# Kernel tuning notes

Measured on AMD Instinct MI355X. Metric: run time of the kernel, lower is better.

Reference implementation:

```python
import jax, jax.numpy as jnp
import numpy as np

N = 100000      # nodes
E = 1600000     # edges (avg degree 16)
IN_DIM = 64
H = 4           # num_heads
D = 32          # out_dim per head
NEG_SLOPE = 0.1


def setup_inputs() -> dict:
    key = jax.random.key(0)
    k_x, k_src, k_dst, k_w, k_fc, k_al, k_ar = jax.random.split(key, 7)
    x = jax.random.normal(k_x, (N, IN_DIM), dtype=jnp.float32)
    src = jax.random.randint(k_src, (E,), 0, N, dtype=jnp.int32)
    dst = jax.random.randint(k_dst, (E,), 0, N, dtype=jnp.int32)
    w = jax.random.uniform(k_w, (E,), dtype=jnp.float32)
    # xavier-ish init for learned params
    W_fc = jax.random.normal(k_fc, (IN_DIM, H * D), dtype=jnp.float32) * (2.0 / (IN_DIM + H * D)) ** 0.5
    attn_l = jax.random.normal(k_al, (1, H, D), dtype=jnp.float32) * 0.1
    attn_r = jax.random.normal(k_ar, (1, H, D), dtype=jnp.float32) * 0.1
    vt = jnp.zeros((1,), dtype=jnp.float32)  # unused by forward (as in the source)
    return {"vt": vt, "x": x, "src": src, "dst": dst, "w": w,
            "W_fc": W_fc, "attn_l": attn_l, "attn_r": attn_r}


def reference(vt, x, src, dst, w, W_fc, attn_l, attn_r):
    # node projection: [N, H, D]
    feat = (x @ W_fc).reshape(-1, H, D)
    el = jnp.sum(feat * attn_l, axis=-1)  # [N, H]
    er = jnp.sum(feat * attn_r, axis=-1)  # [N, H]
    # per-edge logits: u_add_v then leaky_relu, scaled by edge weight w
    e = el[src] + er[dst]                                   # [E, H]
    e = jnp.where(e >= 0, e, NEG_SLOPE * e)                 # leaky_relu
    e = w[:, None] * e                                      # [E, H]
    # edge softmax grouped by destination node (numerically stable)
    m = jax.ops.segment_max(e, dst, num_segments=N)         # [N, H]
    ex = jnp.exp(e - m[dst])                                # [E, H]
    den = jax.ops.segment_sum(ex, dst, num_segments=N)      # [N, H]
    a = ex / den[dst]                                       # [E, H]
    # message passing: u_mul_e -> sum over incoming edges
    msg = feat[src] * a[:, :, None]                         # [E, H, D]
    out = jax.ops.segment_sum(msg, dst, num_segments=N)     # [N, H, D]
    return out
```

## Files before the change

### kernel.cpp

```cpp
#include <hip/hip_runtime.h>
#include <math.h>

#define IN_DIM 64
#define HH 4
#define CC 128
#define NEG_SLOPE 0.1f

typedef __attribute__((ext_vector_type(8))) short short8;
typedef __attribute__((ext_vector_type(4))) float f32x4;

__device__ __forceinline__ float leaky(float v) { return v >= 0.f ? v : NEG_SLOPE * v; }

__device__ __forceinline__ unsigned f2bf(float f) {
  unsigned u = __float_as_uint(f);
  unsigned r = u + 0x7FFFu + ((u >> 16) & 1u);
  return r >> 16;
}

__global__ void k_prepw(const float* __restrict__ W, unsigned* __restrict__ wt) {
  int tid = blockIdx.x * 256 + threadIdx.x;
  if (tid >= 128 * 32) return;
  int n = tid >> 5;
  int r = tid & 31;
  int b = r >> 2, h = r & 3;
  int k = b * 8 + h * 2;
  unsigned lo = f2bf(W[k * CC + n]);
  unsigned hi = f2bf(W[(k + 1) * CC + n]);
  wt[n * 32 + (b ^ (n & 7)) * 4 + h] = lo | (hi << 16);
}

__global__ __launch_bounds__(256) void k_project(
    const float* __restrict__ x, const unsigned* __restrict__ wt,
    const float* __restrict__ attn_l, const float* __restrict__ attn_r,
    unsigned char* __restrict__ featQ, float* __restrict__ scale,
    float* __restrict__ el, float* __restrict__ er, int N)
{
  __shared__ unsigned Wlds[4096];
  __shared__ float Al[CC], Ar[CC];
  int t = threadIdx.x;
  {
    const uint4* s = (const uint4*)wt;
    uint4* d = (uint4*)Wlds;
#pragma unroll
    for (int i = 0; i < 4; ++i) d[t + 256 * i] = s[t + 256 * i];
  }
  if (t < CC) { Al[t] = attn_l[t]; Ar[t] = attn_r[t]; }
  __syncthreads();

  int lane = t & 63;
  int l4 = lane >> 4, l16 = lane & 15;
  int node = blockIdx.x * 64 + (t >> 6) * 16 + l16;
  bool valid = node < N;
  int nrow = valid ? node : 0;

  short8 bfr[2];
#pragma unroll
  for (int s = 0; s < 2; ++s) {
    const float4* xp = (const float4*)&x[(size_t)nrow * 64 + s * 32 + l4 * 8];
    float4 xa = xp[0], xb = xp[1];
    union { short8 v; unsigned u[4]; } pk;
    pk.u[0] = f2bf(xa.x) | (f2bf(xa.y) << 16);
    pk.u[1] = f2bf(xa.z) | (f2bf(xa.w) << 16);
    pk.u[2] = f2bf(xb.x) | (f2bf(xb.y) << 16);
    pk.u[3] = f2bf(xb.z) | (f2bf(xb.w) << 16);
    bfr[s] = pk.v;
  }

  f32x4 acc[8];
#pragma unroll
  for (int c = 0; c < 8; ++c) acc[c] = (f32x4){0.f, 0.f, 0.f, 0.f};

#pragma unroll
  for (int c = 0; c < 8; ++c) {
    int n0 = c * 16 + l16;
    int sw = n0 & 7;
#pragma unroll
    for (int s = 0; s < 2; ++s) {
      int b = s * 4 + l4;
      union { short8 v; uint4 q; } af;
      af.q = *(const uint4*)&Wlds[n0 * 32 + (b ^ sw) * 4];
      acc[c] = __builtin_amdgcn_mfma_f32_16x16x32_bf16(af.v, bfr[s], acc[c], 0, 0, 0);
    }
  }

  float mx = 0.f;
#pragma unroll
  for (int c = 0; c < 8; ++c) {
#pragma unroll
    for (int r = 0; r < 4; ++r) mx = fmaxf(mx, fabsf(acc[c][r]));
  }
  mx = fmaxf(mx, __shfl_xor(mx, 16, 64));
  mx = fmaxf(mx, __shfl_xor(mx, 32, 64));
  float mxs = fmaxf(mx, 1e-20f);
  float inv = 127.f / mxs;

  if (valid) {
#pragma unroll
    for (int c = 0; c < 8; ++c) {
      int q0 = __float2int_rn(acc[c][0] * inv) + 128;
      int q1 = __float2int_rn(acc[c][1] * inv) + 128;
      int q2 = __float2int_rn(acc[c][2] * inv) + 128;
      int q3 = __float2int_rn(acc[c][3] * inv) + 128;
      unsigned u = (unsigned)(q0 & 0xff) | ((unsigned)(q1 & 0xff) << 8) |
                   ((unsigned)(q2 & 0xff) << 16) | ((unsigned)(q3 & 0xff) << 24);
      *(unsigned*)&featQ[(size_t)node * 128 + c * 16 + l4 * 4] = u;
    }
    if (l4 == 0) scale[node] = mxs * (1.f / 127.f);
  }

  float pl[4], pr[4];
#pragma unroll
  for (int h = 0; h < 4; ++h) {
    float sl = 0.f, sr = 0.f;
#pragma unroll
    for (int ct = 0; ct < 2; ++ct) {
      int c = 2 * h + ct;
      int cb = c * 16 + l4 * 4;
#pragma unroll
      for (int r = 0; r < 4; ++r) {
        sl = fmaf(acc[c][r], Al[cb + r], sl);
        sr = fmaf(acc[c][r], Ar[cb + r], sr);
      }
    }
    sl += __shfl_xor(sl, 16, 64); sl += __shfl_xor(sl, 32, 64);
    sr += __shfl_xor(sr, 16, 64); sr += __shfl_xor(sr, 32, 64);
    pl[h] = sl; pr[h] = sr;
  }
  if (l4 == 0 && valid) {
    *(float4*)&el[(size_t)node * 4] = make_float4(pl[0], pl[1], pl[2], pl[3]);
    *(float4*)&er[(size_t)node * 4] = make_float4(pr[0], pr[1], pr[2], pr[3]);
  }
}

__global__ __launch_bounds__(256) void k_bhist(const int* __restrict__ dst,
                                               int* __restrict__ bcnt, int E, int NB) {
  __shared__ int lh[512];
  for (int i = threadIdx.x; i < NB; i += 256) lh[i] = 0;
  __syncthreads();
  int stride = gridDim.x * 256;
  for (int i = blockIdx.x * 256 + threadIdx.x; i < E; i += stride)
    atomicAdd(&lh[dst[i] >> 8], 1);
  __syncthreads();
  for (int i = threadIdx.x; i < NB; i += 256) {
    int c = lh[i];
    if (c) atomicAdd(&bcnt[i], c);
  }
}

__global__ __launch_bounds__(512) void k_bscan(const int* __restrict__ bcnt,
                                               int* __restrict__ gbase,
                                               int* __restrict__ gcursor, int NB) {
  __shared__ int sh[512];
  int t = threadIdx.x;
  int v = (t < NB) ? bcnt[t] : 0;
  sh[t] = v;
  __syncthreads();
  for (int off = 1; off < 512; off <<= 1) {
    int a = (t >= off) ? sh[t - off] : 0;
    __syncthreads();
    sh[t] += a;
    __syncthreads();
  }
  if (t < NB) {
    int e = sh[t] - v;
    gbase[t] = e;
    gcursor[t] = e;
  }
}

__global__ __launch_bounds__(512) void k_binA(const int* __restrict__ src,
                                              const int* __restrict__ dst,
                                              const float* __restrict__ w,
                                              int* __restrict__ gcursor,
                                              uint2* __restrict__ bkt, int E, int NB) {
  __shared__ int lh[512];
  __shared__ int lbase[512];
  int t = threadIdx.x;
  for (int i = t; i < NB; i += 512) lh[i] = 0;
  __syncthreads();
  long eb = (long)blockIdx.x * 8192;
  int b[16]; int r[16]; unsigned px[16]; unsigned pw[16];
#pragma unroll
  for (int i = 0; i < 16; ++i) {
    long e = eb + t + i * 512;
    bool v = e < E;
    int d = v ? dst[e] : 0;
    b[i] = d >> 8;
    px[i] = v ? ((unsigned)src[e] | ((unsigned)(d & 255) << 20)) : 0u;
    pw[i] = v ? ((const unsigned*)w)[e] : 0u;
    r[i] = v ? atomicAdd(&lh[b[i]], 1) : -1;
  }
  __syncthreads();
  for (int i = t; i < NB; i += 512) {
    int c = lh[i];
    lbase[i] = c ? atomicAdd(&gcursor[i], c) : 0;
  }
  __syncthreads();
#pragma unroll
  for (int i = 0; i < 16; ++i)
    if (r[i] >= 0) bkt[lbase[b[i]] + r[i]] = make_uint2(px[i], pw[i]);
}

__global__ __launch_bounds__(256) void k_binB(const uint2* __restrict__ bkt,
                                              const int* __restrict__ bcnt,
                                              const int* __restrict__ gbase,
                                              int* __restrict__ offs,
                                              int2* __restrict__ sp,
                                              int N, int E, int NB) {
  __shared__ int lh[256], sc[256], lcur[256];
  int b = blockIdx.x;
  int t = threadIdx.x;
  int base_b = gbase[b];
  int cnt_b = bcnt[b];
  lh[t] = 0;
  __syncthreads();
  for (int e = t; e < cnt_b; e += 256) {
    uint2 p = bkt[base_b + e];
    atomicAdd(&lh[(p.x >> 20) & 255], 1);
  }
  __syncthreads();
  int v = lh[t];
  sc[t] = v;
  __syncthreads();
  for (int off = 1; off < 256; off <<= 1) {
    int a = (t >= off) ? sc[t - off] : 0;
    __syncthreads();
    sc[t] += a;
    __syncthreads();
  }
  int excl = sc[t] - v;
  lcur[t] = excl;
  int n0 = b << 8;
  if (n0 + t < N) offs[n0 + t] = base_b + excl;
  if (b == NB - 1 && t == 0) offs[N] = E;
  __syncthreads();
  for (int e = t; e < cnt_b; e += 256) {
    uint2 p = bkt[base_b + e];
    int d = (p.x >> 20) & 255;
    int pos = atomicAdd(&lcur[d], 1);
    sp[base_b + pos] = make_int2((int)(p.x & 0xFFFFFu), (int)p.y);
  }
}

__device__ __forceinline__ void fma16(float* acc, float& ka, float a, uint4 f) {
  ka += a;
  acc[0]  = fmaf(a, (float)( f.x        & 0xffu), acc[0]);
  acc[1]  = fmaf(a, (float)((f.x >> 8 ) & 0xffu), acc[1]);
  acc[2]  = fmaf(a, (float)((f.x >> 16) & 0xffu), acc[2]);
  acc[3]  = fmaf(a, (float)( f.x >> 24        ), acc[3]);
  acc[4]  = fmaf(a, (float)( f.y        & 0xffu), acc[4]);
  acc[5]  = fmaf(a, (float)((f.y >> 8 ) & 0xffu), acc[5]);
  acc[6]  = fmaf(a, (float)((f.y >> 16) & 0xffu), acc[6]);
  acc[7]  = fmaf(a, (float)( f.y >> 24        ), acc[7]);
  acc[8]  = fmaf(a, (float)( f.z        & 0xffu), acc[8]);
  acc[9]  = fmaf(a, (float)((f.z >> 8 ) & 0xffu), acc[9]);
  acc[10] = fmaf(a, (float)((f.z >> 16) & 0xffu), acc[10]);
  acc[11] = fmaf(a, (float)( f.z >> 24        ), acc[11]);
  acc[12] = fmaf(a, (float)( f.w        & 0xffu), acc[12]);
  acc[13] = fmaf(a, (float)((f.w >> 8 ) & 0xffu), acc[13]);
  acc[14] = fmaf(a, (float)((f.w >> 16) & 0xffu), acc[14]);
  acc[15] = fmaf(a, (float)( f.w >> 24        ), acc[15]);
}

__global__ __launch_bounds__(256) void k_aggregate(
    const int* __restrict__ offs, const int2* __restrict__ sp,
    const float* __restrict__ el, const float* __restrict__ er,
    const float* __restrict__ scale, const unsigned char* __restrict__ featQ,
    float* __restrict__ out, int N)
{
  __shared__ int    s_lds[4][64];
  __shared__ float4 a_lds[4][64];

  int t = threadIdx.x;
  int lane = t & 63, wv = t >> 6;
  int half = lane >> 5, l32 = lane & 31;
  int n = blockIdx.x * 8 + wv * 2 + half;
  if (n >= N) return;

  int off0 = offs[n], off1 = offs[n + 1];
  int deg = off1 - off0;
  int grp = l32 >> 3;
  int c8 = l32 & 7;
  int hh = c8 >> 1;
  int hlane = lane & 32;
  const unsigned char* featl = featQ + c8 * 16;
  int* slf = &s_lds[wv][half * 32];
  const float* al = (const float*)&a_lds[wv][half * 32];

  float acc[16];
#pragma unroll
  for (int i = 0; i < 16; ++i) acc[i] = 0.f;
  float ka = 0.f;

  if (deg > 0) {
    float4 erv = *reinterpret_cast<const float4*>(&er[(size_t)n * HH]);
    if (deg <= 32) {
      int dm1 = deg - 1;
      bool act = l32 < deg;
      int2 p = sp[off0 + (act ? l32 : 0)];
      int s = p.x;
      float wgt = __int_as_float(p.y);
      float sc = scale[s];

      uint4 fb[8];
#pragma unroll
      for (int k = 0; k < 4; ++k) {
        int ic = 4 * k + grp;
        int icc = ic < dm1 ? ic : dm1;
        int ss = __shfl(s, hlane + icc, 64);
        fb[k] = *reinterpret_cast<const uint4*>(featl + ((size_t)ss << 7));
      }
      if (deg > 16) {
#pragma unroll
        for (int k = 4; k < 8; ++k) {
          int ic = 4 * k + grp;
          int icc = ic < dm1 ? ic : dm1;
          int ss = __shfl(s, hlane + icc, 64);
          fb[k] = *reinterpret_cast<const uint4*>(featl + ((size_t)ss << 7));
        }
      }

      float4 elv = *reinterpret_cast<const float4*>(&el[(size_t)s * HH]);
      float x0 = act ? __expf(leaky(elv.x + erv.x) * wgt) : 0.f;
      float x1 = act ? __expf(leaky(elv.y + erv.y) * wgt) : 0.f;
      float x2 = act ? __expf(leaky(elv.z + erv.z) * wgt) : 0.f;
      float x3 = act ? __expf(leaky(elv.w + erv.w) * wgt) : 0.f;
      float d0 = x0, d1 = x1, d2 = x2, d3 = x3;
#pragma unroll
      for (int d = 16; d >= 1; d >>= 1) {
        d0 += __shfl_xor(d0, d, 64);
        d1 += __shfl_xor(d1, d, 64);
        d2 += __shfl_xor(d2, d, 64);
        d3 += __shfl_xor(d3, d, 64);
      }
      float a0 = x0 * __builtin_amdgcn_rcpf(d0) * sc;
      float a1 = x1 * __builtin_amdgcn_rcpf(d1) * sc;
      float a2 = x2 * __builtin_amdgcn_rcpf(d2) * sc;
      float a3 = x3 * __builtin_amdgcn_rcpf(d3) * sc;
      a_lds[wv][half * 32 + l32] = make_float4(a0, a1, a2, a3);

#pragma unroll
      for (int k = 0; k < 4; ++k) {
        int ic = 4 * k + grp;
        int icc = ic < dm1 ? ic : dm1;
        float a = (ic < deg) ? al[icc * 4 + hh] : 0.f;
        fma16(acc, ka, a, fb[k]);
      }
      if (deg > 16) {
#pragma unroll
        for (int k = 4; k < 8; ++k) {
          int ic = 4 * k + grp;
          int icc = ic < dm1 ? ic : dm1;
          float a = (ic < deg) ? al[icc * 4 + hh] : 0.f;
          fma16(acc, ka, a, fb[k]);
        }
      }
    } else {
      float m0 = -INFINITY, m1 = -INFINITY, m2 = -INFINITY, m3 = -INFINITY;
      for (int base = off0; base < off1; base += 32) {
        int j = base + l32;
        bool act = j < off1;
        int2 p = sp[act ? j : off0];
        float wgt = __int_as_float(p.y);
        float4 elv = *reinterpret_cast<const float4*>(&el[(size_t)p.x * HH]);
        float e0 = act ? leaky(elv.x + erv.x) * wgt : -INFINITY;
        float e1 = act ? leaky(elv.y + erv.y) * wgt : -INFINITY;
        float e2 = act ? leaky(elv.z + erv.z) * wgt : -INFINITY;
        float e3 = act ? leaky(elv.w + erv.w) * wgt : -INFINITY;
        m0 = fmaxf(m0, e0); m1 = fmaxf(m1, e1);
        m2 = fmaxf(m2, e2); m3 = fmaxf(m3, e3);
      }
#pragma unroll
      for (int d = 16; d >= 1; d >>= 1) {
        m0 = fmaxf(m0, __shfl_xor(m0, d, 64));
        m1 = fmaxf(m1, __shfl_xor(m1, d, 64));
        m2 = fmaxf(m2, __shfl_xor(m2, d, 64));
        m3 = fmaxf(m3, __shfl_xor(m3, d, 64));
      }
      float d0 = 0.f, d1 = 0.f, d2 = 0.f, d3 = 0.f;
      for (int base = off0; base < off1; base += 32) {
        int j = base + l32;
        bool act = j < off1;
        int2 p = sp[act ? j : off0];
        float wgt = __int_as_float(p.y);
        float4 elv = *reinterpret_cast<const float4*>(&el[(size_t)p.x * HH]);
        d0 += act ? __expf(leaky(elv.x + erv.x) * wgt - m0) : 0.f;
        d1 += act ? __expf(leaky(elv.y + erv.y) * wgt - m1) : 0.f;
        d2 += act ? __expf(leaky(elv.z + erv.z) * wgt - m2) : 0.f;
        d3 += act ? __expf(leaky(elv.w + erv.w) * wgt - m3) : 0.f;
      }
#pragma unroll
      for (int d = 16; d >= 1; d >>= 1) {
        d0 += __shfl_xor(d0, d, 64);
        d1 += __shfl_xor(d1, d, 64);
        d2 += __shfl_xor(d2, d, 64);
        d3 += __shfl_xor(d3, d, 64);
      }
      float i0 = __builtin_amdgcn_rcpf(d0), i1 = __builtin_amdgcn_rcpf(d1);
      float i2 = __builtin_amdgcn_rcpf(d2), i3 = __builtin_amdgcn_rcpf(d3);
      for (int base = off0; base < off1; base += 32) {
        int j = base + l32;
        bool act = j < off1;
        int2 p = sp[act ? j : off0];
        float wgt = __int_as_float(p.y);
        float sc = scale[p.x];
        float4 elv = *reinterpret_cast<const float4*>(&el[(size_t)p.x * HH]);
        float a0 = act ? __expf(leaky(elv.x + erv.x) * wgt - m0) * i0 * sc : 0.f;
        float a1 = act ? __expf(leaky(elv.y + erv.y) * wgt - m1) * i1 * sc : 0.f;
        float a2 = act ? __expf(leaky(elv.z + erv.z) * wgt - m2) * i2 * sc : 0.f;
        float a3 = act ? __expf(leaky(elv.w + erv.w) * wgt - m3) * i3 * sc : 0.f;
        slf[l32] = p.x << 7;
        a_lds[wv][half * 32 + l32] = make_float4(a0, a1, a2, a3);
        int cnt = off1 - base; if (cnt > 32) cnt = 32;
        int ne2 = (cnt + 3) >> 2;
        for (int b0 = 0; b0 < ne2; b0 += 4) {
          uint4 fb[4];
          float av[4];
#pragma unroll
          for (int k = 0; k < 4; ++k) {
            int idx = 4 * (b0 + k) + grp;
            bool vv = idx < cnt;
            int ic = vv ? idx : 0;
            av[k] = vv ? al[ic * 4 + hh] : 0.f;
            fb[k] = *reinterpret_cast<const uint4*>(featl + slf[ic]);
          }
#pragma unroll
          for (int k = 0; k < 4; ++k) fma16(acc, ka, av[k], fb[k]);
        }
      }
    }
  }
#pragma unroll
  for (int d = 8; d <= 16; d <<= 1) {
#pragma unroll
    for (int i = 0; i < 16; ++i) acc[i] += __shfl_xor(acc[i], d, 64);
    ka += __shfl_xor(ka, d, 64);
  }
  if (grp == 0) {
    float base = 128.f * ka;
    float* orow = &out[(size_t)n * CC + c8 * 16];
#pragma unroll
    for (int k = 0; k < 4; ++k) {
      f32x4 o = {acc[4 * k] - base, acc[4 * k + 1] - base,
                 acc[4 * k + 2] - base, acc[4 * k + 3] - base};
      *reinterpret_cast<f32x4*>(orow + 4 * k) = o;
    }
  }
}

extern "C" void kernel_launch(void* const* d_in, const int* in_sizes, int n_in,
                              void* d_out, int out_size, void* d_ws, size_t ws_size,
                              hipStream_t stream)
{
  const float* x      = (const float*)d_in[1];
  const int*   src    = (const int*)d_in[2];
  const int*   dst    = (const int*)d_in[3];
  const float* w      = (const float*)d_in[4];
  const float* W_fc   = (const float*)d_in[5];
  const float* attn_l = (const float*)d_in[6];
  const float* attn_r = (const float*)d_in[7];
  float* out = (float*)d_out;

  int N = in_sizes[1] / IN_DIM;
  int E = in_sizes[2];
  int NB = (N + 255) / 256;

  char* p = (char*)d_ws;
  auto alloc = [&](size_t bytes) {
    char* r = p;
    p += (bytes + 255) & ~size_t(255);
    return r;
  };
  unsigned char* featQ = (unsigned char*)alloc((size_t)N * 128);
  float* scale = (float*)alloc((size_t)N * 4);
  float* el    = (float*)alloc((size_t)N * HH * 4);
  float* er    = (float*)alloc((size_t)N * HH * 4);
  int*   offs  = (int*)alloc((size_t)(N + 1) * 4);
  int*   bcnt  = (int*)alloc(512 * 4);
  int*   gbase = (int*)alloc(512 * 4);
  int*   gcur  = (int*)alloc(512 * 4);
  unsigned* wtswz = (unsigned*)alloc(4096 * 4);
  uint2* bkt   = (uint2*)alloc((size_t)E * 8);
  int2*  sp    = (int2*)alloc((size_t)E * 8);

  hipMemsetAsync(bcnt, 0, 512 * 4, stream);

  k_prepw<<<16, 256, 0, stream>>>(W_fc, wtswz);
  k_project<<<(N + 63) / 64, 256, 0, stream>>>(x, wtswz, attn_l, attn_r,
                                               featQ, scale, el, er, N);
  k_bhist<<<256, 256, 0, stream>>>(dst, bcnt, E, NB);
  k_bscan<<<1, 512, 0, stream>>>(bcnt, gbase, gcur, NB);
  k_binA<<<(E + 8191) / 8192, 512, 0, stream>>>(src, dst, w, gcur, bkt, E, NB);
  k_binB<<<NB, 256, 0, stream>>>(bkt, bcnt, gbase, offs, sp, N, E, NB);
  k_aggregate<<<(N + 7) / 8, 256, 0, stream>>>(offs, sp, el, er, scale, featQ, out, N);
}
```

Before: 134.2 us.

## Fuse weight prep and histogram into projection; persistent aggregate with nontemporal stores

The separate weight-swizzle kernel is removed: each projection block now converts and swizzles W_fc into LDS itself. The destination-bucket histogram blocks are appended to the projection grid so both run in one launch. The aggregation kernel becomes a grid-stride persistent kernel capped at 2048 blocks, and its output writes use nontemporal stores. Together these cut two launches and some per-block overhead, at the cost of every projection block redundantly converting all of W from global memory.

```diff
diff --git a/kernel.cpp b/kernel.cpp
--- a/kernel.cpp
+++ b/kernel.cpp
@@ -17,32 +17,42 @@
   return r >> 16;
 }
 
-__global__ void k_prepw(const float* __restrict__ W, unsigned* __restrict__ wt) {
-  int tid = blockIdx.x * 256 + threadIdx.x;
-  if (tid >= 128 * 32) return;
-  int n = tid >> 5;
-  int r = tid & 31;
-  int b = r >> 2, h = r & 3;
-  int k = b * 8 + h * 2;
-  unsigned lo = f2bf(W[k * CC + n]);
-  unsigned hi = f2bf(W[(k + 1) * CC + n]);
-  wt[n * 32 + (b ^ (n & 7)) * 4 + h] = lo | (hi << 16);
-}
-
-__global__ __launch_bounds__(256) void k_project(
-    const float* __restrict__ x, const unsigned* __restrict__ wt,
+__global__ __launch_bounds__(256) void k_projhist(
+    const float* __restrict__ x, const float* __restrict__ W,
     const float* __restrict__ attn_l, const float* __restrict__ attn_r,
     unsigned char* __restrict__ featQ, float* __restrict__ scale,
-    float* __restrict__ el, float* __restrict__ er, int N)
+    float* __restrict__ el, float* __restrict__ er,
+    const int* __restrict__ dst, int* __restrict__ bcnt,
+    int N, int E, int NB, int projB)
 {
   __shared__ unsigned Wlds[4096];
   __shared__ float Al[CC], Ar[CC];
+  __shared__ int lh[512];
   int t = threadIdx.x;
-  {
-    const uint4* s = (const uint4*)wt;
-    uint4* d = (uint4*)Wlds;
-#pragma unroll
-    for (int i = 0; i < 4; ++i) d[t + 256 * i] = s[t + 256 * i];
+
+  if ((int)blockIdx.x >= projB) {
+    int hb = blockIdx.x - projB;
+    for (int i = t; i < NB; i += 256) lh[i] = 0;
+    __syncthreads();
+    for (int i = hb * 256 + t; i < E; i += 256 * 256)
+      atomicAdd(&lh[dst[i] >> 8], 1);
+    __syncthreads();
+    for (int i = t; i < NB; i += 256) {
+      int c = lh[i];
+      if (c) atomicAdd(&bcnt[i], c);
+    }
+    return;
+  }
+
+#pragma unroll
+  for (int i = 0; i < 16; ++i) {
+    int idx = t + 256 * i;
+    int nn = idx >> 5, r = idx & 31;
+    int bb = r >> 2, h2 = r & 3;
+    int kk = bb * 8 + h2 * 2;
+    unsigned lo = f2bf(W[kk * CC + nn]);
+    unsigned hi = f2bf(W[(kk + 1) * CC + nn]);
+    Wlds[nn * 32 + (bb ^ (nn & 7)) * 4 + h2] = lo | (hi << 16);
   }
   if (t < CC) { Al[t] = attn_l[t]; Ar[t] = attn_r[t]; }
   __syncthreads();
@@ -129,21 +139,6 @@
   if (l4 == 0 && valid) {
     *(float4*)&el[(size_t)node * 4] = make_float4(pl[0], pl[1], pl[2], pl[3]);
     *(float4*)&er[(size_t)node * 4] = make_float4(pr[0], pr[1], pr[2], pr[3]);
-  }
-}
-
-__global__ __launch_bounds__(256) void k_bhist(const int* __restrict__ dst,
-                                               int* __restrict__ bcnt, int E, int NB) {
-  __shared__ int lh[512];
-  for (int i = threadIdx.x; i < NB; i += 256) lh[i] = 0;
-  __syncthreads();
-  int stride = gridDim.x * 256;
-  for (int i = blockIdx.x * 256 + threadIdx.x; i < E; i += stride)
-    atomicAdd(&lh[dst[i] >> 8], 1);
-  __syncthreads();
-  for (int i = threadIdx.x; i < NB; i += 256) {
-    int c = lh[i];
-    if (c) atomicAdd(&bcnt[i], c);
   }
 }
 
@@ -266,7 +261,7 @@
     const int* __restrict__ offs, const int2* __restrict__ sp,
     const float* __restrict__ el, const float* __restrict__ er,
     const float* __restrict__ scale, const unsigned char* __restrict__ featQ,
-    float* __restrict__ out, int N)
+    float* __restrict__ out, int ngroups, int N)
 {
   __shared__ int    s_lds[4][64];
   __shared__ float4 a_lds[4][64];
@@ -274,11 +269,6 @@
   int t = threadIdx.x;
   int lane = t & 63, wv = t >> 6;
   int half = lane >> 5, l32 = lane & 31;
-  int n = blockIdx.x * 8 + wv * 2 + half;
-  if (n >= N) return;
-
-  int off0 = offs[n], off1 = offs[n + 1];
-  int deg = off1 - off0;
   int grp = l32 >> 3;
   int c8 = l32 & 7;
   int hh = c8 >> 1;
@@ -287,163 +277,171 @@
   int* slf = &s_lds[wv][half * 32];
   const float* al = (const float*)&a_lds[wv][half * 32];
 
-  float acc[16];
-#pragma unroll
-  for (int i = 0; i < 16; ++i) acc[i] = 0.f;
-  float ka = 0.f;
-
-  if (deg > 0) {
-    float4 erv = *reinterpret_cast<const float4*>(&er[(size_t)n * HH]);
-    if (deg <= 32) {
-      int dm1 = deg - 1;
-      bool act = l32 < deg;
-      int2 p = sp[off0 + (act ? l32 : 0)];
-      int s = p.x;
-      float wgt = __int_as_float(p.y);
-      float sc = scale[s];
-
-      uint4 fb[8];
-#pragma unroll
-      for (int k = 0; k < 4; ++k) {
-        int ic = 4 * k + grp;
-        int icc = ic < dm1 ? ic : dm1;
-        int ss = __shfl(s, hlane + icc, 64);
-        fb[k] = *reinterpret_cast<const uint4*>(featl + ((size_t)ss << 7));
-      }
-      if (deg > 16) {
-#pragma unroll
-        for (int k = 4; k < 8; ++k) {
+  for (int g = blockIdx.x; g < ngroups; g += gridDim.x) {
+    int n = g * 8 + wv * 2 + half;
+    if (n >= N) continue;
+
+    int off0 = offs[n], off1 = offs[n + 1];
+    int deg = off1 - off0;
+
+    float acc[16];
+#pragma unroll
+    for (int i = 0; i < 16; ++i) acc[i] = 0.f;
+    float ka = 0.f;
+
+    if (deg > 0) {
+      float4 erv = *reinterpret_cast<const float4*>(&er[(size_t)n * HH]);
+      if (deg <= 32) {
+        int dm1 = deg - 1;
+        bool act = l32 < deg;
+        int2 p = sp[off0 + (act ? l32 : 0)];
+        int s = p.x;
+        float wgt = __int_as_float(p.y);
+        float sc = scale[s];
+
+        uint4 fb[8];
+#pragma unroll
+        for (int k = 0; k < 4; ++k) {
           int ic = 4 * k + grp;
           int icc = ic < dm1 ? ic : dm1;
           int ss = __shfl(s, hlane + icc, 64);
           fb[k] = *reinterpret_cast<const uint4*>(featl + ((size_t)ss << 7));
         }
-      }
-
-      float4 elv = *reinterpret_cast<const float4*>(&el[(size_t)s * HH]);
-      float x0 = act ? __expf(leaky(elv.x + erv.x) * wgt) : 0.f;
-      float x1 = act ? __expf(leaky(elv.y + erv.y) * wgt) : 0.f;
-      float x2 = act ? __expf(leaky(elv.z + erv.z) * wgt) : 0.f;
-      float x3 = act ? __expf(leaky(elv.w + erv.w) * wgt) : 0.f;
-      float d0 = x0, d1 = x1, d2 = x2, d3 = x3;
-#pragma unroll
-      for (int d = 16; d >= 1; d >>= 1) {
-        d0 += __shfl_xor(d0, d, 64);
-        d1 += __shfl_xor(d1, d, 64);
-        d2 += __shfl_xor(d2, d, 64);
-        d3 += __shfl_xor(d3, d, 64);
-      }
-      float a0 = x0 * __builtin_amdgcn_rcpf(d0) * sc;
-      float a1 = x1 * __builtin_amdgcn_rcpf(d1) * sc;
-      float a2 = x2 * __builtin_amdgcn_rcpf(d2) * sc;
-      float a3 = x3 * __builtin_amdgcn_rcpf(d3) * sc;
-      a_lds[wv][half * 32 + l32] = make_float4(a0, a1, a2, a3);
-
-#pragma unroll
-      for (int k = 0; k < 4; ++k) {
-        int ic = 4 * k + grp;
-        int icc = ic < dm1 ? ic : dm1;
-        float a = (ic < deg) ? al[icc * 4 + hh] : 0.f;
-        fma16(acc, ka, a, fb[k]);
-      }
-      if (deg > 16) {
-#pragma unroll
-        for (int k = 4; k < 8; ++k) {
+        if (deg > 16) {
+#pragma unroll
+          for (int k = 4; k < 8; ++k) {
+            int ic = 4 * k + grp;
+            int icc = ic < dm1 ? ic : dm1;
+            int ss = __shfl(s, hlane + icc, 64);
+            fb[k] = *reinterpret_cast<const uint4*>(featl + ((size_t)ss << 7));
+          }
+        }
+
+        float4 elv = *reinterpret_cast<const float4*>(&el[(size_t)s * HH]);
+        float x0 = act ? __expf(leaky(elv.x + erv.x) * wgt) : 0.f;
+        float x1 = act ? __expf(leaky(elv.y + erv.y) * wgt) : 0.f;
+        float x2 = act ? __expf(leaky(elv.z + erv.z) * wgt) : 0.f;
+        float x3 = act ? __expf(leaky(elv.w + erv.w) * wgt) : 0.f;
+        float d0 = x0, d1 = x1, d2 = x2, d3 = x3;
+#pragma unroll
+        for (int d = 16; d >= 1; d >>= 1) {
+          d0 += __shfl_xor(d0, d, 64);
+          d1 += __shfl_xor(d1, d, 64);
+          d2 += __shfl_xor(d2, d, 64);
+          d3 += __shfl_xor(d3, d, 64);
+        }
+        float a0 = x0 * __builtin_amdgcn_rcpf(d0) * sc;
+        float a1 = x1 * __builtin_amdgcn_rcpf(d1) * sc;
+        float a2 = x2 * __builtin_amdgcn_rcpf(d2) * sc;
+        float a3 = x3 * __builtin_amdgcn_rcpf(d3) * sc;
+        a_lds[wv][half * 32 + l32] = make_float4(a0, a1, a2, a3);
+
+#pragma unroll
+        for (int k = 0; k < 4; ++k) {
           int ic = 4 * k + grp;
           int icc = ic < dm1 ? ic : dm1;
           float a = (ic < deg) ? al[icc * 4 + hh] : 0.f;
           fma16(acc, ka, a, fb[k]);
         }
+        if (deg > 16) {
+#pragma unroll
+          for (int k = 4; k < 8; ++k) {
+            int ic = 4 * k + grp;
+            int icc = ic < dm1 ? ic : dm1;
+            float a = (ic < deg) ? al[icc * 4 + hh] : 0.f;
+            fma16(acc, ka, a, fb[k]);
+          }
+        }
+      } else {
+        float m0 = -INFINITY, m1 = -INFINITY, m2 = -INFINITY, m3 = -INFINITY;
+        for (int base = off0; base < off1; base += 32) {
+          int j = base + l32;
+          bool act = j < off1;
+          int2 p = sp[act ? j : off0];
+          float wgt = __int_as_float(p.y);
+          float4 elv = *reinterpret_cast<const float4*>(&el[(size_t)p.x * HH]);
+          float e0 = act ? leaky(elv.x + erv.x) * wgt : -INFINITY;
+          float e1 = act ? leaky(elv.y + erv.y) * wgt : -INFINITY;
+          float e2 = act ? leaky(elv.z + erv.z) * wgt : -INFINITY;
+          float e3 = act ? leaky(elv.w + erv.w) * wgt : -INFINITY;
+          m0 = fmaxf(m0, e0); m1 = fmaxf(m1, e1);
+          m2 = fmaxf(m2, e2); m3 = fmaxf(m3, e3);
+        }
+#pragma unroll
+        for (int d = 16; d >= 1; d >>= 1) {
+          m0 = fmaxf(m0, __shfl_xor(m0, d, 64));
+          m1 = fmaxf(m1, __shfl_xor(m1, d, 64));
+          m2 = fmaxf(m2, __shfl_xor(m2, d, 64));
+          m3 = fmaxf(m3, __shfl_xor(m3, d, 64));
+        }
+        float d0 = 0.f, d1 = 0.f, d2 = 0.f, d3 = 0.f;
+        for (int base = off0; base < off1; base += 32) {
+          int j = base + l32;
+          bool act = j < off1;
+          int2 p = sp[act ? j : off0];
+          float wgt = __int_as_float(p.y);
+          float4 elv = *reinterpret_cast<const float4*>(&el[(size_t)p.x * HH]);
+          d0 += act ? __expf(leaky(elv.x + erv.x) * wgt - m0) : 0.f;
+          d1 += act ? __expf(leaky(elv.y + erv.y) * wgt - m1) : 0.f;
+          d2 += act ? __expf(leaky(elv.z + erv.z) * wgt - m2) : 0.f;
+          d3 += act ? __expf(leaky(elv.w + erv.w) * wgt - m3) : 0.f;
+        }
+#pragma unroll
+        for (int d = 16; d >= 1; d >>= 1) {
+          d0 += __shfl_xor(d0, d, 64);
+          d1 += __shfl_xor(d1, d, 64);
+          d2 += __shfl_xor(d2, d, 64);
+          d3 += __shfl_xor(d3, d, 64);
+        }
+        float i0 = __builtin_amdgcn_rcpf(d0), i1 = __builtin_amdgcn_rcpf(d1);
+        float i2 = __builtin_amdgcn_rcpf(d2), i3 = __builtin_amdgcn_rcpf(d3);
+        for (int base = off0; base < off1; base += 32) {
+          int j = base + l32;
+          bool act = j < off1;
+          int2 p = sp[act ? j : off0];
+          float wgt = __int_as_float(p.y);
+          float sc = scale[p.x];
+          float4 elv = *reinterpret_cast<const float4*>(&el[(size_t)p.x * HH]);
+          float a0 = act ? __expf(leaky(elv.x + erv.x) * wgt - m0) * i0 * sc : 0.f;
+          float a1 = act ? __expf(leaky(elv.y + erv.y) * wgt - m1) * i1 * sc : 0.f;
+          float a2 = act ? __expf(leaky(elv.z + erv.z) * wgt - m2) * i2 * sc : 0.f;
+          float a3 = act ? __expf(leaky(elv.w + erv.w) * wgt - m3) * i3 * sc : 0.f;
+          slf[l32] = p.x << 7;
+          a_lds[wv][half * 32 + l32] = make_float4(a0, a1, a2, a3);
+          int cnt = off1 - base; if (cnt > 32) cnt = 32;
+          int ne2 = (cnt + 3) >> 2;
+          for (int b0 = 0; b0 < ne2; b0 += 4) {
+            uint4 fb[4];
+            float av[4];
+#pragma unroll
+            for (int k = 0; k < 4; ++k) {
+              int idx = 4 * (b0 + k) + grp;
+              bool vv = idx < cnt;
+              int ic = vv ? idx : 0;
+              av[k] = vv ? al[ic * 4 + hh] : 0.f;
+              fb[k] = *reinterpret_cast<const uint4*>(featl + slf[ic]);
+            }
+#pragma unroll
+            for (int k = 0; k < 4; ++k) fma16(acc, ka, av[k], fb[k]);
+          }
+        }
       }
-    } else {
-      float m0 = -INFINITY, m1 = -INFINITY, m2 = -INFINITY, m3 = -INFINITY;
-      for (int base = off0; base < off1; base += 32) {
-        int j = base + l32;
-        bool act = j < off1;
-        int2 p = sp[act ? j : off0];
-        float wgt = __int_as_float(p.y);
-        float4 elv = *reinterpret_cast<const float4*>(&el[(size_t)p.x * HH]);
-        float e0 = act ? leaky(elv.x + erv.x) * wgt : -INFINITY;
-        float e1 = act ? leaky(elv.y + erv.y) * wgt : -INFINITY;
-        float e2 = act ? leaky(elv.z + erv.z) * wgt : -INFINITY;
-        float e3 = act ? leaky(elv.w + erv.w) * wgt : -INFINITY;
-        m0 = fmaxf(m0, e0); m1 = fmaxf(m1, e1);
-        m2 = fmaxf(m2, e2); m3 = fmaxf(m3, e3);
+    }
+#pragma unroll
+    for (int d = 8; d <= 16; d <<= 1) {
+#pragma unroll
+      for (int i = 0; i < 16; ++i) acc[i] += __shfl_xor(acc[i], d, 64);
+      ka += __shfl_xor(ka, d, 64);
+    }
+    if (grp == 0) {
+      float base = 128.f * ka;
+      float* orow = &out[(size_t)n * CC + c8 * 16];
+#pragma unroll
+      for (int k = 0; k < 4; ++k) {
+        f32x4 o = {acc[4 * k] - base, acc[4 * k + 1] - base,
+                   acc[4 * k + 2] - base, acc[4 * k + 3] - base};
+        __builtin_nontemporal_store(o, reinterpret_cast<f32x4*>(orow + 4 * k));
       }
-#pragma unroll
-      for (int d = 16; d >= 1; d >>= 1) {
-        m0 = fmaxf(m0, __shfl_xor(m0, d, 64));
-        m1 = fmaxf(m1, __shfl_xor(m1, d, 64));
-        m2 = fmaxf(m2, __shfl_xor(m2, d, 64));
-        m3 = fmaxf(m3, __shfl_xor(m3, d, 64));
-      }
-      float d0 = 0.f, d1 = 0.f, d2 = 0.f, d3 = 0.f;
-      for (int base = off0; base < off1; base += 32) {
-        int j = base + l32;
-        bool act = j < off1;
-        int2 p = sp[act ? j : off0];
-        float wgt = __int_as_float(p.y);
-        float4 elv = *reinterpret_cast<const float4*>(&el[(size_t)p.x * HH]);
-        d0 += act ? __expf(leaky(elv.x + erv.x) * wgt - m0) : 0.f;
-        d1 += act ? __expf(leaky(elv.y + erv.y) * wgt - m1) : 0.f;
-        d2 += act ? __expf(leaky(elv.z + erv.z) * wgt - m2) : 0.f;
-        d3 += act ? __expf(leaky(elv.w + erv.w) * wgt - m3) : 0.f;
-      }
-#pragma unroll
-      for (int d = 16; d >= 1; d >>= 1) {
-        d0 += __shfl_xor(d0, d, 64);
-        d1 += __shfl_xor(d1, d, 64);
-        d2 += __shfl_xor(d2, d, 64);
-        d3 += __shfl_xor(d3, d, 64);
-      }
-      float i0 = __builtin_amdgcn_rcpf(d0), i1 = __builtin_amdgcn_rcpf(d1);
-      float i2 = __builtin_amdgcn_rcpf(d2), i3 = __builtin_amdgcn_rcpf(d3);
-      for (int base = off0; base < off1; base += 32) {
-        int j = base + l32;
-        bool act = j < off1;
-        int2 p = sp[act ? j : off0];
-        float wgt = __int_as_float(p.y);
-        float sc = scale[p.x];
-        float4 elv = *reinterpret_cast<const float4*>(&el[(size_t)p.x * HH]);
-        float a0 = act ? __expf(leaky(elv.x + erv.x) * wgt - m0) * i0 * sc : 0.f;
-        float a1 = act ? __expf(leaky(elv.y + erv.y) * wgt - m1) * i1 * sc : 0.f;
-        float a2 = act ? __expf(leaky(elv.z + erv.z) * wgt - m2) * i2 * sc : 0.f;
-        float a3 = act ? __expf(leaky(elv.w + erv.w) * wgt - m3) * i3 * sc : 0.f;
-        slf[l32] = p.x << 7;
-        a_lds[wv][half * 32 + l32] = make_float4(a0, a1, a2, a3);
-        int cnt = off1 - base; if (cnt > 32) cnt = 32;
-        int ne2 = (cnt + 3) >> 2;
-        for (int b0 = 0; b0 < ne2; b0 += 4) {
-          uint4 fb[4];
-          float av[4];
-#pragma unroll
-          for (int k = 0; k < 4; ++k) {
-            int idx = 4 * (b0 + k) + grp;
-            bool vv = idx < cnt;
-            int ic = vv ? idx : 0;
-            av[k] = vv ? al[ic * 4 + hh] : 0.f;
-            fb[k] = *reinterpret_cast<const uint4*>(featl + slf[ic]);
-          }
-#pragma unroll
-          for (int k = 0; k < 4; ++k) fma16(acc, ka, av[k], fb[k]);
-        }
-      }
-    }
-  }
-#pragma unroll
-  for (int d = 8; d <= 16; d <<= 1) {
-#pragma unroll
-    for (int i = 0; i < 16; ++i) acc[i] += __shfl_xor(acc[i], d, 64);
-    ka += __shfl_xor(ka, d, 64);
-  }
-  if (grp == 0) {
-    float base = 128.f * ka;
-    float* orow = &out[(size_t)n * CC + c8 * 16];
-#pragma unroll
-    for (int k = 0; k < 4; ++k) {
-      f32x4 o = {acc[4 * k] - base, acc[4 * k + 1] - base,
-                 acc[4 * k + 2] - base, acc[4 * k + 3] - base};
-      *reinterpret_cast<f32x4*>(orow + 4 * k) = o;
     }
   }
 }
@@ -479,18 +477,21 @@
   int*   bcnt  = (int*)alloc(512 * 4);
   int*   gbase = (int*)alloc(512 * 4);
   int*   gcur  = (int*)alloc(512 * 4);
-  unsigned* wtswz = (unsigned*)alloc(4096 * 4);
   uint2* bkt   = (uint2*)alloc((size_t)E * 8);
   int2*  sp    = (int2*)alloc((size_t)E * 8);
 
   hipMemsetAsync(bcnt, 0, 512 * 4, stream);
 
-  k_prepw<<<16, 256, 0, stream>>>(W_fc, wtswz);
-  k_project<<<(N + 63) / 64, 256, 0, stream>>>(x, wtswz, attn_l, attn_r,
-                                               featQ, scale, el, er, N);
-  k_bhist<<<256, 256, 0, stream>>>(dst, bcnt, E, NB);
+  int projB = (N + 63) / 64;
+  k_projhist<<<projB + 256, 256, 0, stream>>>(x, W_fc, attn_l, attn_r,
+                                              featQ, scale, el, er,
+                                              dst, bcnt, N, E, NB, projB);
   k_bscan<<<1, 512, 0, stream>>>(bcnt, gbase, gcur, NB);
   k_binA<<<(E + 8191) / 8192, 512, 0, stream>>>(src, dst, w, gcur, bkt, E, NB);
   k_binB<<<NB, 256, 0, stream>>>(bkt, bcnt, gbase, offs, sp, N, E, NB);
-  k_aggregate<<<(N + 7) / 8, 256, 0, stream>>>(offs, sp, el, er, scale, featQ, out, N);
-}
+
+  int ngroups = (N + 7) / 8;
+  int agrid = ngroups < 2048 ? ngroups : 2048;
+  k_aggregate<<<agrid, 256, 0, stream>>>(offs, sp, el, er, scale, featQ, out,
+                                         ngroups, N);
+}
```

Result: slower. 154.9 us (+15.4%).
